# Kernel optimization log

Measured on AMD Instinct MI355X. Metric: run time of the kernel, lower is better.

Reference implementation:

```python
import jax, jax.numpy as jnp
import numpy as np

BLKQ = 64
BLKK = 64
TOPK_RATIO = 0.125


def setup_inputs() -> dict:
    key = jax.random.key(0)
    ks = jax.random.split(key, 4)
    B, L, H, D = 1, 4096, 16, 64
    q = jax.random.normal(ks[0], (B, L, H, D), jnp.float32)
    k = jax.random.normal(ks[1], (B, L, H, D), jnp.float32)
    v = jax.random.normal(ks[2], (B, L, H, D), jnp.float32)
    w_proj = jax.random.normal(ks[3], (D, D), jnp.float32) * 0.02
    b_proj = jnp.zeros((D,), jnp.float32)
    return {"q": q, "k": k, "v": v, "w_proj": w_proj, "b_proj": b_proj}


def _sparse_linear_attn(q, k, v, w_proj, b_proj):
    # q,k,v: (B, L, H, D) -> (B, H, L, D)
    q = jnp.transpose(q, (0, 2, 1, 3))
    k = jnp.transpose(k, (0, 2, 1, 3))
    v = jnp.transpose(v, (0, 2, 1, 3))
    B, H, L, D = q.shape
    M, N = L // BLKQ, L // BLKK  # L chosen divisible by block sizes (no padding)
    T = max(1, int(TOPK_RATIO * N))  # selected key blocks per query block

    qb = q.reshape(B, H, M, BLKQ, D)
    kb = k.reshape(B, H, N, BLKK, D)
    vb = v.reshape(B, H, N, BLKK, D)

    # --- block map: mean-pooled block descriptors, topk key blocks per query block ---
    qm = qb.mean(axis=3)  # (B,H,M,D)
    km = kb.mean(axis=3)  # (B,H,N,D)
    blk_scores = jnp.einsum('bhmd,bhnd->bhmn', qm, km)
    _, lut = jax.lax.top_k(blk_scores, T)  # (B,H,M,T) int32

    # --- gather selected K/V blocks ---
    b_idx = jnp.arange(B)[:, None, None, None]
    h_idx = jnp.arange(H)[None, :, None, None]
    k_sel = kb[b_idx, h_idx, lut]  # (B,H,M,T,BLKK,D)
    v_sel = vb[b_idx, h_idx, lut]  # (B,H,M,T,BLKK,D)

    # --- block-sparse softmax attention over gathered keys only ---
    scale = D ** (-0.5)
    att = jnp.einsum('bhmqd,bhmtkd->bhmqtk', qb, k_sel) * scale
    att = att.reshape(B, H, M, BLKQ, T * BLKK)
    p = jax.nn.softmax(att, axis=-1)
    o_s = jnp.einsum('bhmqn,bhmnd->bhmqd', p, v_sel.reshape(B, H, M, T * BLKK, D))
    o_s = o_s.reshape(B, H, L, D)

    # --- global linear attention with softmax feature map ---
    q_fm = jax.nn.softmax(q, axis=-1)
    k_fm = jax.nn.softmax(k, axis=-1)
    kvsum = jnp.einsum('bhld,bhle->bhde', k_fm, v)  # (B,H,D,D)
    ksum = k_fm.sum(axis=2)  # (B,H,D)
    num = jnp.einsum('bhld,bhde->bhle', q_fm, kvsum)
    den = jnp.einsum('bhld,bhd->bhl', q_fm, ksum)[..., None] + 1e-6
    o_l = num / den
    o_l = jnp.einsum('bhld,ed->bhle', o_l, w_proj) + b_proj  # nn.Linear: x @ W.T + b

    o = o_s + o_l
    return jnp.transpose(o, (0, 2, 1, 3))  # (B, L, H, D)


def reference(q, k, v, w_proj, b_proj):
    return _sparse_linear_attn(q, k, v, w_proj, b_proj)
```

## Files before the change

kernel.cpp:

```cpp
#include <hip/hip_runtime.h>


#define NH   16
#define DH   64
#define NBLK 64
#define TSEL 8

typedef unsigned short u16;
typedef unsigned int   u32;
typedef __attribute__((ext_vector_type(8))) short short8;
typedef __attribute__((ext_vector_type(4))) float f4;

#define MFMA_BF16(a, b, c) __builtin_amdgcn_mfma_f32_16x16x32_bf16(a, b, c, 0, 0, 0)

__device__ __forceinline__ u16 f2bf_rne(float f) {
  u32 u = __float_as_uint(f);
  u += 0x7fffu + ((u >> 16) & 1u);
  return (u16)(u >> 16);
}
__device__ __forceinline__ u32 pk2(float a, float b) {
  return (u32)f2bf_rne(a) | ((u32)f2bf_rne(b) << 16);
}
__device__ __forceinline__ float bf2f(u16 u) { return __uint_as_float(((u32)u) << 16); }

__device__ __forceinline__ short8 frag_row(const u16* t, int row, int jblk) {
  return *(const short8*)((const char*)t + row * 128 + ((jblk ^ (row & 7)) * 16));
}

__global__ __launch_bounds__(256) void prep_kernel(const float* __restrict__ q,
                                                   const float* __restrict__ k,
                                                   const float* __restrict__ v,
                                                   u16* __restrict__ kT,
                                                   u16* __restrict__ vT,
                                                   float* __restrict__ kvsum,
                                                   float* __restrict__ ksum,
                                                   float* __restrict__ kmv,
                                                   float* __restrict__ qkp) {
  __shared__ __align__(16) char vsl[8192];
  __shared__ __align__(16) char kfm[8192];
  __shared__ float redmx[256];
  __shared__ float redsm[256];
  __shared__ float ksred[256];
  int n = blockIdx.x, h = blockIdx.y, tid = threadIdx.x;
  int w = tid >> 6, lane = tid & 63;
  int row = lane, qd = w;
  int lq = lane & 15, quad = lane >> 4;

  float kv[16];
  {
    const float* kr = k + (size_t)(n * 64 + row) * 1024 + h * 64 + qd * 16;
#pragma unroll
    for (int c4 = 0; c4 < 4; c4++) {
      float4 a = *(const float4*)(kr + c4 * 4);
      kv[c4 * 4] = a.x; kv[c4 * 4 + 1] = a.y; kv[c4 * 4 + 2] = a.z; kv[c4 * 4 + 3] = a.w;
    }
  }
  {
    char* ktb = (char*)(kT + ((size_t)(h * 64 + n)) * 4096);
    uint4 w0 = make_uint4(pk2(kv[0], kv[1]), pk2(kv[2], kv[3]),
                          pk2(kv[4], kv[5]), pk2(kv[6], kv[7]));
    uint4 w1 = make_uint4(pk2(kv[8], kv[9]), pk2(kv[10], kv[11]),
                          pk2(kv[12], kv[13]), pk2(kv[14], kv[15]));
    *(uint4*)(ktb + row * 128 + (((2 * qd) ^ (row & 7)) * 16)) = w0;
    *(uint4*)(ktb + row * 128 + (((2 * qd + 1) ^ (row & 7)) * 16)) = w1;
  }
  {
    const float* vr = v + (size_t)(n * 64 + row) * 1024 + h * 64 + qd * 16;
    int kb = row >> 3, klo = row & 7;
#pragma unroll
    for (int c4 = 0; c4 < 4; c4++) {
      float4 a = *(const float4*)(vr + c4 * 4);
      float vv[4] = {a.x, a.y, a.z, a.w};
#pragma unroll
      for (int jj = 0; jj < 4; jj++) {
        int e = qd * 16 + c4 * 4 + jj;
        *(u16*)(vsl + e * 128 + ((kb ^ (e & 7)) * 16) + klo * 2) = f2bf_rne(vv[jj]);
      }
    }
  }
  {
    float kmval = 0.f;
#pragma unroll
    for (int j = 0; j < 16; j++) {
      float s = kv[j];
#pragma unroll
      for (int off = 1; off < 64; off <<= 1) s += __shfl_xor(s, off);
      if (lane == j) kmval = s;
    }
    if (lane < 16) kmv[h * 4096 + n * 64 + qd * 16 + lane] = kmval * (1.0f / 64.0f);
  }
  {
    float mx = kv[0];
#pragma unroll
    for (int j = 1; j < 16; j++) mx = fmaxf(mx, kv[j]);
    redmx[qd * 64 + row] = mx;
  }
  __syncthreads();
  {
    float mx = fmaxf(fmaxf(redmx[row], redmx[64 + row]),
                     fmaxf(redmx[128 + row], redmx[192 + row]));
    float sm = 0.f;
#pragma unroll
    for (int j = 0; j < 16; j++) { kv[j] = __expf(kv[j] - mx); sm += kv[j]; }
    redsm[qd * 64 + row] = sm;
  }
  __syncthreads();
  {
    float sm = redsm[row] + redsm[64 + row] + redsm[128 + row] + redsm[192 + row];
    float inv = 1.0f / sm;
    int rb = row >> 3, rlo = row & 7;
#pragma unroll
    for (int j = 0; j < 16; j++) {
      int d = qd * 16 + j;
      *(u16*)(kfm + d * 128 + (((rb) ^ (d & 7)) * 16) + rlo * 2) = f2bf_rne(kv[j] * inv);
    }
  }
  __syncthreads();

  {
    uint4* vt_out = (uint4*)(vT + ((size_t)(h * 64 + n)) * 4096);
    vt_out[tid] = ((const uint4*)vsl)[tid];
    vt_out[256 + tid] = ((const uint4*)vsl)[256 + tid];
  }
  {
    float ks = 0.f;
    short8 x0 = frag_row((const u16*)kfm, lane, 2 * w);
    short8 x1 = frag_row((const u16*)kfm, lane, 2 * w + 1);
#pragma unroll
    for (int e = 0; e < 8; e++) ks += bf2f((u16)x0[e]) + bf2f((u16)x1[e]);
    ksred[tid] = ks;
  }
  {
    f4 acc[4];
    f4 zz = {0.f, 0.f, 0.f, 0.f};
#pragma unroll
    for (int et = 0; et < 4; et++) acc[et] = zz;
#pragma unroll
    for (int ks2 = 0; ks2 < 2; ks2++) {
      short8 a_ = frag_row((const u16*)kfm, w * 16 + lq, 4 * ks2 + quad);
#pragma unroll
      for (int et = 0; et < 4; et++)
        acc[et] = MFMA_BF16(a_, frag_row((const u16*)vsl, et * 16 + lq, 4 * ks2 + quad), acc[et]);
    }
#pragma unroll
    for (int et = 0; et < 4; et++)
#pragma unroll
      for (int r = 0; r < 4; r++)
        atomicAdd(&kvsum[h * 4096 + (w * 16 + quad * 4 + r) * 64 + et * 16 + lq],
                  acc[et][r]);
  }
  __syncthreads();
  if (tid < 64)
    atomicAdd(&ksum[h * 64 + tid], ksred[tid] + ksred[64 + tid] +
                                   ksred[128 + tid] + ksred[192 + tid]);

  if (h < 4) {
    const float* base = q + ((size_t)(n * 64 + h * 16)) * 1024 + tid * 4;
    float4 acc = {0.f, 0.f, 0.f, 0.f};
#pragma unroll
    for (int i = 0; i < 16; i++) {
      float4 a = *(const float4*)(base + (size_t)i * 1024);
      acc.x += a.x; acc.y += a.y; acc.z += a.z; acc.w += a.w;
    }
    *(float4*)(qkp + ((size_t)(h * 64 + n)) * 1024 + tid * 4) = acc;
  }
}

__global__ __launch_bounds__(256) void post_kernel(const float* __restrict__ qkp,
                                                   const float* __restrict__ kmv,
                                                   const float* __restrict__ kvsum,
                                                   const float* __restrict__ wgt,
                                                   int* __restrict__ lut,
                                                   u16* __restrict__ m2t) {
  __shared__ float kv_s[64 * 65];
  __shared__ float w_s[64 * 65];
  __shared__ __align__(16) float qr_s[4][80];
  int bx = blockIdx.x, tid = threadIdx.x;
  if (bx < 256) {
    int h = bx >> 4, w = tid >> 6, n = tid & 63;
    int m = (bx & 15) * 4 + w;
    float qsum = 0.f;
#pragma unroll
    for (int rs = 0; rs < 4; rs++)
      qsum += qkp[((size_t)(rs * 64 + m)) * 1024 + h * 64 + n];
    qr_s[w][n] = qsum;
    __syncthreads();
    const float* kr = kmv + h * 4096 + n * 64;
    float s = 0.f;
#pragma unroll
    for (int d = 0; d < 64; d += 4) {
      float4 a = *(const float4*)(kr + d);
      float4 b = *(const float4*)(&qr_s[w][d]);
      s += a.x * b.x + a.y * b.y + a.z * b.z + a.w * b.w;
    }
    float my = s;
    for (int t = 0; t < TSEL; t++) {
      float v = my; int idx = n;
#pragma unroll
      for (int off = 1; off < 64; off <<= 1) {
        float ov = __shfl_xor(v, off);
        int oi = __shfl_xor(idx, off);
        if (ov > v || (ov == v && oi < idx)) { v = ov; idx = oi; }
      }
      if (n == 0) lut[(h * NBLK + m) * TSEL + t] = idx;
      if (n == idx) my = -INFINITY;
    }
  } else {
    int h = bx - 256;
#pragma unroll
    for (int jj = 0; jj < 16; jj++) {
      int idx = jj * 256 + tid;
      kv_s[(idx >> 6) * 65 + (idx & 63)] = kvsum[h * 4096 + idx];
      w_s[(idx >> 6) * 65 + (idx & 63)] = wgt[idx];
    }
    __syncthreads();
    int d = tid >> 2, e0 = (tid & 3) * 16;
    float acc[16];
#pragma unroll
    for (int e = 0; e < 16; e++) acc[e] = 0.f;
    for (int j = 0; j < 64; j++) {
      float kvj = kv_s[d * 65 + j];
#pragma unroll
      for (int e = 0; e < 16; e++)
        acc[e] = fmaf(kvj, w_s[(e0 + e) * 65 + j], acc[e]);
    }
    char* base = (char*)m2t + (size_t)h * 8192;
#pragma unroll
    for (int e = 0; e < 16; e++) {
      int ee = e0 + e;
      *(u16*)(base + ee * 128 + (((d >> 3) ^ (ee & 7)) * 16) + (d & 7) * 2) = f2bf_rne(acc[e]);
    }
  }
}

__global__ __launch_bounds__(256, 4) void fused_attn_kernel(const float* __restrict__ q,
                                                            const u16* __restrict__ kT,
                                                            const u16* __restrict__ vT,
                                                            const int* __restrict__ lut,
                                                            const u16* __restrict__ m2t,
                                                            const float* __restrict__ ksum,
                                                            const float* __restrict__ bproj,
                                                            float* __restrict__ out) {
  __shared__ __align__(16) char smem[33280];
  int m = blockIdx.x, h = blockIdx.y;
  int tid = threadIdx.x, w = tid >> 6, lane = tid & 63;
  int lq = lane & 15, quad = lane >> 4;
  u16* q_l = (u16*)smem;
  char* buf = smem + 8192;
  char* p_b = smem + 24576 + w * 2048;
  float* ks_s = (float*)(smem + 32768);
  float* b_s = (float*)(smem + 33024);

  const int lb = (h * NBLK + m) * TSEL;
  int blks[8];
#pragma unroll
  for (int t = 0; t < 8; t++) blks[t] = lut[lb + t];

  {
#pragma unroll
    for (int c = 0; c < 2; c++) {
      int lo = c * 4096 + tid * 16;
      int r = lo >> 7;
      int j = ((lo >> 4) & 7) ^ (r & 7);
      const float* gp = q + ((size_t)(m * 64 + r)) * 1024 + h * 64 + j * 8;
      float4 a = *(const float4*)gp;
      float4 b = *(const float4*)(gp + 4);
      *(uint4*)(smem + lo) = make_uint4(pk2(a.x, a.y), pk2(a.z, a.w),
                                        pk2(b.x, b.y), pk2(b.z, b.w));
    }
  }
  {
    const uint4* kt0 = (const uint4*)(kT + ((size_t)(h * 64 + blks[0])) * 4096);
    const uint4* vt0 = (const uint4*)(vT + ((size_t)(h * 64 + blks[0])) * 4096);
    ((uint4*)buf)[tid] = kt0[tid];
    ((uint4*)buf)[256 + tid] = kt0[256 + tid];
    ((uint4*)(buf + 8192))[tid] = vt0[tid];
    ((uint4*)(buf + 8192))[256 + tid] = vt0[256 + tid];
    if (tid < 64) { ks_s[tid] = ksum[h * 64 + tid]; b_s[tid] = bproj[tid]; }
  }
  __syncthreads();

  const int qrow = w * 16 + lq;
  short8 qf[2];
#pragma unroll
  for (int ks = 0; ks < 2; ks++) qf[ks] = frag_row(q_l, qrow, 4 * ks + quad);

  float mrun = -INFINITY, lrun = 0.f;
  f4 o[4];
  f4 zz = {0.f, 0.f, 0.f, 0.f};
#pragma unroll
  for (int et = 0; et < 4; et++) o[et] = zz;

  const u16* kc = (const u16*)buf;
  const u16* vc = (const u16*)(buf + 8192);

  for (int t = 0; t < 8; t++) {
    uint4 pk0, pk1, pv0, pv1;
    if (t < 7) {
      const uint4* ktn = (const uint4*)(kT + ((size_t)(h * 64 + blks[t + 1])) * 4096);
      const uint4* vtn = (const uint4*)(vT + ((size_t)(h * 64 + blks[t + 1])) * 4096);
      pk0 = ktn[tid]; pk1 = ktn[256 + tid];
      pv0 = vtn[tid]; pv1 = vtn[256 + tid];
    }

    f4 s[4];
#pragma unroll
    for (int kt = 0; kt < 4; kt++) s[kt] = zz;
#pragma unroll
    for (int ks = 0; ks < 2; ks++)
#pragma unroll
      for (int kt = 0; kt < 4; kt++)
        s[kt] = MFMA_BF16(frag_row(kc, kt * 16 + lq, 4 * ks + quad), qf[ks], s[kt]);

    float mp = -INFINITY;
#pragma unroll
    for (int kt = 0; kt < 4; kt++)
#pragma unroll
      for (int r = 0; r < 4; r++) mp = fmaxf(mp, s[kt][r]);
    mp = fmaxf(mp, __shfl_xor(mp, 16));
    mp = fmaxf(mp, __shfl_xor(mp, 32));
    mp *= 0.125f;
    float mn = fmaxf(mrun, mp);
    float al = __expf(mrun - mn);
    mrun = mn;
    float rs_ = 0.f;
#pragma unroll
    for (int kt = 0; kt < 4; kt++) {
      float p0 = __expf(fmaf(s[kt][0], 0.125f, -mn));
      float p1 = __expf(fmaf(s[kt][1], 0.125f, -mn));
      float p2 = __expf(fmaf(s[kt][2], 0.125f, -mn));
      float p3 = __expf(fmaf(s[kt][3], 0.125f, -mn));
      rs_ += p0 + p1 + p2 + p3;
      u32 lo32 = (__float_as_uint(p0) >> 16) | (__float_as_uint(p1) & 0xffff0000u);
      u32 hi32 = (__float_as_uint(p2) >> 16) | (__float_as_uint(p3) & 0xffff0000u);
      int addr = lq * 128 + (((kt * 2 + (quad >> 1)) ^ (lq & 7)) * 16) + (quad & 1) * 8;
      *(uint2*)(p_b + addr) = make_uint2(lo32, hi32);
    }
    rs_ += __shfl_xor(rs_, 16);
    rs_ += __shfl_xor(rs_, 32);
    lrun = lrun * al + rs_;
#pragma unroll
    for (int et = 0; et < 4; et++)
#pragma unroll
      for (int r = 0; r < 4; r++) o[et][r] *= al;

#pragma unroll
    for (int ks = 0; ks < 2; ks++) {
      short8 pf = frag_row((const u16*)p_b, lq, 4 * ks + quad);
#pragma unroll
      for (int et = 0; et < 4; et++)
        o[et] = MFMA_BF16(frag_row(vc, et * 16 + lq, 4 * ks + quad), pf, o[et]);
    }

    if (t < 7) {
      __syncthreads();
      ((uint4*)buf)[tid] = pk0;
      ((uint4*)buf)[256 + tid] = pk1;
      ((uint4*)(buf + 8192))[tid] = pv0;
      ((uint4*)(buf + 8192))[256 + tid] = pv1;
      __syncthreads();
    }
  }

  __syncthreads();
  {
    const uint4* src = (const uint4*)((const char*)m2t + (size_t)h * 8192);
    ((uint4*)buf)[tid] = src[tid];
    ((uint4*)buf)[256 + tid] = src[256 + tid];
  }
  __syncthreads();
  u16* m2_l = (u16*)buf;

  short8 qa = frag_row(q_l, qrow, 2 * quad);
  short8 qb = frag_row(q_l, qrow, 2 * quad + 1);
  float ev[16];
  float mx = -INFINITY;
#pragma unroll
  for (int j = 0; j < 8; j++) { float x = bf2f((u16)qa[j]); ev[j] = x; mx = fmaxf(mx, x); }
#pragma unroll
  for (int j = 0; j < 8; j++) { float x = bf2f((u16)qb[j]); ev[8 + j] = x; mx = fmaxf(mx, x); }
  mx = fmaxf(mx, __shfl_xor(mx, 16));
  mx = fmaxf(mx, __shfl_xor(mx, 32));
  float sum = 0.f, eks = 0.f;
#pragma unroll
  for (int j = 0; j < 16; j++) {
    float e = __expf(ev[j] - mx);
    ev[j] = e;
    sum += e;
    eks += e * ks_s[quad * 16 + j];
  }
  sum += __shfl_xor(sum, 16); sum += __shfl_xor(sum, 32);
  eks += __shfl_xor(eks, 16); eks += __shfl_xor(eks, 32);
  float invs = 1.0f / sum;
  float den = fmaf(eks, invs, 1e-6f);
  float scale = invs / den;
  uint4 e0v = make_uint4(pk2(ev[0], ev[1]), pk2(ev[2], ev[3]),
                         pk2(ev[4], ev[5]), pk2(ev[6], ev[7]));
  uint4 e1v = make_uint4(pk2(ev[8], ev[9]), pk2(ev[10], ev[11]),
                         pk2(ev[12], ev[13]), pk2(ev[14], ev[15]));
  *(uint4*)(p_b + lq * 128 + (((2 * quad) ^ (lq & 7)) * 16)) = e0v;
  *(uint4*)(p_b + lq * 128 + (((2 * quad + 1) ^ (lq & 7)) * 16)) = e1v;

  f4 oc[4];
#pragma unroll
  for (int et = 0; et < 4; et++) oc[et] = zz;
#pragma unroll
  for (int ks2 = 0; ks2 < 2; ks2++) {
    short8 ef = frag_row((const u16*)p_b, lq, 4 * ks2 + quad);
#pragma unroll
    for (int et = 0; et < 4; et++)
      oc[et] = MFMA_BF16(frag_row(m2_l, et * 16 + lq, 4 * ks2 + quad), ef, oc[et]);
  }

  float invl = 1.0f / lrun;
  float* gp = out + ((size_t)(m * 64 + qrow)) * 1024 + h * 64 + quad * 4;
#pragma unroll
  for (int et = 0; et < 4; et++) {
    int e0 = et * 16 + quad * 4;
    float4 ov;
    ov.x = o[et][0] * invl + oc[et][0] * scale + b_s[e0 + 0];
    ov.y = o[et][1] * invl + oc[et][1] * scale + b_s[e0 + 1];
    ov.z = o[et][2] * invl + oc[et][2] * scale + b_s[e0 + 2];
    ov.w = o[et][3] * invl + oc[et][3] * scale + b_s[e0 + 3];
    *(float4*)(gp + et * 16) = ov;
  }
}

extern "C" void kernel_launch(void* const* d_in, const int* in_sizes, int n_in,
                              void* d_out, int out_size, void* d_ws, size_t ws_size,
                              hipStream_t stream) {
  const float* q = (const float*)d_in[0];
  const float* k = (const float*)d_in[1];
  const float* v = (const float*)d_in[2];
  const float* w = (const float*)d_in[3];
  const float* b = (const float*)d_in[4];
  float* out = (float*)d_out;

  u16* kT = (u16*)d_ws;
  u16* vT = kT + 4194304;
  float* qkp = (float*)(vT + 4194304);
  float* kmv = qkp + 262144;
  int* lut = (int*)(kmv + 65536);
  float* kvsum = (float*)(lut + 8192);
  float* ksum = kvsum + 65536;
  u16* m2t = (u16*)(ksum + 1024);

  hipMemsetAsync(kvsum, 0, (65536 + 1024) * sizeof(float), stream);
  prep_kernel<<<dim3(64, 16), 256, 0, stream>>>(q, k, v, kT, vT, kvsum, ksum, kmv, qkp);
  post_kernel<<<272, 256, 0, stream>>>(qkp, kmv, kvsum, w, lut, m2t);
  fused_attn_kernel<<<dim3(64, 16), 256, 0, stream>>>(q, kT, vT, lut, m2t, ksum, b, out);
}
```

Measured before the change: 154.8 us.

## Rebalance prep/post work, remap block order, lazy softmax rescale, MFMA priority hints

The q-block pooling work, previously done only by blocks with h<4, is now spread across all prep blocks with smaller partial sums, and post reduces more partials. The k-mean shuffle reductions are replaced by an LDS transpose-and-sum. The kvsum×W projection is split across four blocks per head with float4 weight reads. A flat 1D grid with a head/block remap places heads across XCDs. The attention kernel skips the online-softmax rescale when no lane's max increases, wraps its MFMA sections in s_setprio, and trims LDS so it can target five blocks per CU. Together these aim to cut load imbalance, shuffle cost and occupancy limits, at the cost of more partial-sum traffic and extra LDS in prep.

```diff
diff --git a/kernel.cpp b/kernel.cpp
--- a/kernel.cpp
+++ b/kernel.cpp
@@ -35,13 +35,18 @@
                                                    float* __restrict__ kvsum,
                                                    float* __restrict__ ksum,
                                                    float* __restrict__ kmv,
-                                                   float* __restrict__ qkp) {
+                                                   float* __restrict__ qkp2) {
   __shared__ __align__(16) char vsl[8192];
   __shared__ __align__(16) char kfm[8192];
+  __shared__ float kcol[64 * 65];
   __shared__ float redmx[256];
   __shared__ float redsm[256];
+  __shared__ float kmred[256];
   __shared__ float ksred[256];
-  int n = blockIdx.x, h = blockIdx.y, tid = threadIdx.x;
+  int b = blockIdx.x;
+  int n = (b >> 3) & 63;
+  int h = 2 * (b & 7) + (b >> 9);
+  int tid = threadIdx.x;
   int w = tid >> 6, lane = tid & 63;
   int row = lane, qd = w;
   int lq = lane & 15, quad = lane >> 4;
@@ -65,6 +70,10 @@
     *(uint4*)(ktb + row * 128 + (((2 * qd + 1) ^ (row & 7)) * 16)) = w1;
   }
   {
+#pragma unroll
+    for (int j = 0; j < 16; j++) kcol[(qd * 16 + j) * 65 + row] = kv[j];
+  }
+  {
     const float* vr = v + (size_t)(n * 64 + row) * 1024 + h * 64 + qd * 16;
     int kb = row >> 3, klo = row & 7;
 #pragma unroll
@@ -79,23 +88,19 @@
     }
   }
   {
-    float kmval = 0.f;
-#pragma unroll
-    for (int j = 0; j < 16; j++) {
-      float s = kv[j];
-#pragma unroll
-      for (int off = 1; off < 64; off <<= 1) s += __shfl_xor(s, off);
-      if (lane == j) kmval = s;
-    }
-    if (lane < 16) kmv[h * 4096 + n * 64 + qd * 16 + lane] = kmval * (1.0f / 64.0f);
-  }
-  {
     float mx = kv[0];
 #pragma unroll
     for (int j = 1; j < 16; j++) mx = fmaxf(mx, kv[j]);
     redmx[qd * 64 + row] = mx;
   }
   __syncthreads();
+  {
+    int c = tid & 63, g = tid >> 6;
+    float pk = 0.f;
+#pragma unroll
+    for (int i = 0; i < 16; i++) pk += kcol[c * 65 + g * 16 + i];
+    kmred[g * 64 + c] = pk;
+  }
   {
     float mx = fmaxf(fmaxf(redmx[row], redmx[64 + row]),
                      fmaxf(redmx[128 + row], redmx[192 + row]));
@@ -105,6 +110,9 @@
     redsm[qd * 64 + row] = sm;
   }
   __syncthreads();
+  if (tid < 64)
+    kmv[h * 4096 + n * 64 + tid] =
+        (kmred[tid] + kmred[64 + tid] + kmred[128 + tid] + kmred[192 + tid]) * (1.0f / 64.0f);
   {
     float sm = redsm[row] + redsm[64 + row] + redsm[128 + row] + redsm[192 + row];
     float inv = 1.0f / sm;
@@ -154,26 +162,26 @@
     atomicAdd(&ksum[h * 64 + tid], ksred[tid] + ksred[64 + tid] +
                                    ksred[128 + tid] + ksred[192 + tid]);
 
-  if (h < 4) {
-    const float* base = q + ((size_t)(n * 64 + h * 16)) * 1024 + tid * 4;
+  {
+    const float* base = q + ((size_t)(n * 64 + h * 4)) * 1024 + tid * 4;
     float4 acc = {0.f, 0.f, 0.f, 0.f};
 #pragma unroll
-    for (int i = 0; i < 16; i++) {
+    for (int i = 0; i < 4; i++) {
       float4 a = *(const float4*)(base + (size_t)i * 1024);
       acc.x += a.x; acc.y += a.y; acc.z += a.z; acc.w += a.w;
     }
-    *(float4*)(qkp + ((size_t)(h * 64 + n)) * 1024 + tid * 4) = acc;
-  }
-}
-
-__global__ __launch_bounds__(256) void post_kernel(const float* __restrict__ qkp,
+    *(float4*)(qkp2 + ((size_t)(h * 64 + n)) * 1024 + tid * 4) = acc;
+  }
+}
+
+__global__ __launch_bounds__(256) void post_kernel(const float* __restrict__ qkp2,
                                                    const float* __restrict__ kmv,
                                                    const float* __restrict__ kvsum,
                                                    const float* __restrict__ wgt,
                                                    int* __restrict__ lut,
                                                    u16* __restrict__ m2t) {
   __shared__ float kv_s[64 * 65];
-  __shared__ float w_s[64 * 65];
+  __shared__ __align__(16) float wt[64 * 20];
   __shared__ __align__(16) float qr_s[4][80];
   int bx = blockIdx.x, tid = threadIdx.x;
   if (bx < 256) {
@@ -181,8 +189,8 @@
     int m = (bx & 15) * 4 + w;
     float qsum = 0.f;
 #pragma unroll
-    for (int rs = 0; rs < 4; rs++)
-      qsum += qkp[((size_t)(rs * 64 + m)) * 1024 + h * 64 + n];
+    for (int jg = 0; jg < 16; jg++)
+      qsum += qkp2[((size_t)(jg * 64 + m)) * 1024 + h * 64 + n];
     qr_s[w][n] = qsum;
     __syncthreads();
     const float* kr = kmv + h * 4096 + n * 64;
@@ -190,50 +198,55 @@
 #pragma unroll
     for (int d = 0; d < 64; d += 4) {
       float4 a = *(const float4*)(kr + d);
-      float4 b = *(const float4*)(&qr_s[w][d]);
-      s += a.x * b.x + a.y * b.y + a.z * b.z + a.w * b.w;
+      float4 bb = *(const float4*)(&qr_s[w][d]);
+      s += a.x * bb.x + a.y * bb.y + a.z * bb.z + a.w * bb.w;
     }
     float my = s;
     for (int t = 0; t < TSEL; t++) {
-      float v = my; int idx = n;
+      float vv = my; int idx = n;
 #pragma unroll
       for (int off = 1; off < 64; off <<= 1) {
-        float ov = __shfl_xor(v, off);
+        float ov = __shfl_xor(vv, off);
         int oi = __shfl_xor(idx, off);
-        if (ov > v || (ov == v && oi < idx)) { v = ov; idx = oi; }
+        if (ov > vv || (ov == vv && oi < idx)) { vv = ov; idx = oi; }
       }
       if (n == 0) lut[(h * NBLK + m) * TSEL + t] = idx;
       if (n == idx) my = -INFINITY;
     }
   } else {
-    int h = bx - 256;
+    int ib = bx - 256, h = ib >> 2, eq = ib & 3;
 #pragma unroll
     for (int jj = 0; jj < 16; jj++) {
-      int idx = jj * 256 + tid;
-      kv_s[(idx >> 6) * 65 + (idx & 63)] = kvsum[h * 4096 + idx];
-      w_s[(idx >> 6) * 65 + (idx & 63)] = wgt[idx];
+      int id2 = jj * 256 + tid;
+      kv_s[(id2 >> 6) * 65 + (id2 & 63)] = kvsum[h * 4096 + id2];
+    }
+#pragma unroll
+    for (int i = 0; i < 4; i++) {
+      int f = i * 256 + tid;
+      wt[(f & 63) * 20 + (f >> 6)] = wgt[(eq * 16 + (f >> 6)) * 64 + (f & 63)];
     }
     __syncthreads();
-    int d = tid >> 2, e0 = (tid & 3) * 16;
-    float acc[16];
-#pragma unroll
-    for (int e = 0; e < 16; e++) acc[e] = 0.f;
-    for (int j = 0; j < 64; j++) {
-      float kvj = kv_s[d * 65 + j];
-#pragma unroll
-      for (int e = 0; e < 16; e++)
-        acc[e] = fmaf(kvj, w_s[(e0 + e) * 65 + j], acc[e]);
+    int d = tid & 63, g = tid >> 6;
+    float4 acc = {0.f, 0.f, 0.f, 0.f};
+    for (int jj = 0; jj < 64; jj++) {
+      float kvj = kv_s[d * 65 + jj];
+      float4 wv = *(const float4*)(&wt[jj * 20 + g * 4]);
+      acc.x = fmaf(kvj, wv.x, acc.x);
+      acc.y = fmaf(kvj, wv.y, acc.y);
+      acc.z = fmaf(kvj, wv.z, acc.z);
+      acc.w = fmaf(kvj, wv.w, acc.w);
     }
     char* base = (char*)m2t + (size_t)h * 8192;
-#pragma unroll
-    for (int e = 0; e < 16; e++) {
-      int ee = e0 + e;
-      *(u16*)(base + ee * 128 + (((d >> 3) ^ (ee & 7)) * 16) + (d & 7) * 2) = f2bf_rne(acc[e]);
-    }
-  }
-}
-
-__global__ __launch_bounds__(256, 4) void fused_attn_kernel(const float* __restrict__ q,
+    float av[4] = {acc.x, acc.y, acc.z, acc.w};
+#pragma unroll
+    for (int c = 0; c < 4; c++) {
+      int ee = eq * 16 + g * 4 + c;
+      *(u16*)(base + ee * 128 + (((d >> 3) ^ (ee & 7)) * 16) + (d & 7) * 2) = f2bf_rne(av[c]);
+    }
+  }
+}
+
+__global__ __launch_bounds__(256, 5) void fused_attn_kernel(const float* __restrict__ q,
                                                             const u16* __restrict__ kT,
                                                             const u16* __restrict__ vT,
                                                             const int* __restrict__ lut,
@@ -241,15 +254,15 @@
                                                             const float* __restrict__ ksum,
                                                             const float* __restrict__ bproj,
                                                             float* __restrict__ out) {
-  __shared__ __align__(16) char smem[33280];
-  int m = blockIdx.x, h = blockIdx.y;
+  __shared__ __align__(16) char smem[32768];
+  int b = blockIdx.x;
+  int m = (b >> 3) & 63;
+  int h = 2 * (b & 7) + (b >> 9);
   int tid = threadIdx.x, w = tid >> 6, lane = tid & 63;
   int lq = lane & 15, quad = lane >> 4;
   u16* q_l = (u16*)smem;
   char* buf = smem + 8192;
   char* p_b = smem + 24576 + w * 2048;
-  float* ks_s = (float*)(smem + 32768);
-  float* b_s = (float*)(smem + 33024);
 
   const int lb = (h * NBLK + m) * TSEL;
   int blks[8];
@@ -264,9 +277,9 @@
       int j = ((lo >> 4) & 7) ^ (r & 7);
       const float* gp = q + ((size_t)(m * 64 + r)) * 1024 + h * 64 + j * 8;
       float4 a = *(const float4*)gp;
-      float4 b = *(const float4*)(gp + 4);
+      float4 bb = *(const float4*)(gp + 4);
       *(uint4*)(smem + lo) = make_uint4(pk2(a.x, a.y), pk2(a.z, a.w),
-                                        pk2(b.x, b.y), pk2(b.z, b.w));
+                                        pk2(bb.x, bb.y), pk2(bb.z, bb.w));
     }
   }
   {
@@ -276,7 +289,6 @@
     ((uint4*)buf)[256 + tid] = kt0[256 + tid];
     ((uint4*)(buf + 8192))[tid] = vt0[tid];
     ((uint4*)(buf + 8192))[256 + tid] = vt0[256 + tid];
-    if (tid < 64) { ks_s[tid] = ksum[h * 64 + tid]; b_s[tid] = bproj[tid]; }
   }
   __syncthreads();
 
@@ -306,11 +318,13 @@
     f4 s[4];
 #pragma unroll
     for (int kt = 0; kt < 4; kt++) s[kt] = zz;
+    __builtin_amdgcn_s_setprio(1);
 #pragma unroll
     for (int ks = 0; ks < 2; ks++)
 #pragma unroll
       for (int kt = 0; kt < 4; kt++)
         s[kt] = MFMA_BF16(frag_row(kc, kt * 16 + lq, 4 * ks + quad), qf[ks], s[kt]);
+    __builtin_amdgcn_s_setprio(0);
 
     float mp = -INFINITY;
 #pragma unroll
@@ -320,16 +334,23 @@
     mp = fmaxf(mp, __shfl_xor(mp, 16));
     mp = fmaxf(mp, __shfl_xor(mp, 32));
     mp *= 0.125f;
-    float mn = fmaxf(mrun, mp);
-    float al = __expf(mrun - mn);
-    mrun = mn;
+    if (__any(mp > mrun)) {
+      float mn = fmaxf(mrun, mp);
+      float al = __expf(mrun - mn);
+      mrun = mn;
+      lrun *= al;
+#pragma unroll
+      for (int et = 0; et < 4; et++)
+#pragma unroll
+        for (int r = 0; r < 4; r++) o[et][r] *= al;
+    }
     float rs_ = 0.f;
 #pragma unroll
     for (int kt = 0; kt < 4; kt++) {
-      float p0 = __expf(fmaf(s[kt][0], 0.125f, -mn));
-      float p1 = __expf(fmaf(s[kt][1], 0.125f, -mn));
-      float p2 = __expf(fmaf(s[kt][2], 0.125f, -mn));
-      float p3 = __expf(fmaf(s[kt][3], 0.125f, -mn));
+      float p0 = __expf(fmaf(s[kt][0], 0.125f, -mrun));
+      float p1 = __expf(fmaf(s[kt][1], 0.125f, -mrun));
+      float p2 = __expf(fmaf(s[kt][2], 0.125f, -mrun));
+      float p3 = __expf(fmaf(s[kt][3], 0.125f, -mrun));
       rs_ += p0 + p1 + p2 + p3;
       u32 lo32 = (__float_as_uint(p0) >> 16) | (__float_as_uint(p1) & 0xffff0000u);
       u32 hi32 = (__float_as_uint(p2) >> 16) | (__float_as_uint(p3) & 0xffff0000u);
@@ -338,12 +359,9 @@
     }
     rs_ += __shfl_xor(rs_, 16);
     rs_ += __shfl_xor(rs_, 32);
-    lrun = lrun * al + rs_;
-#pragma unroll
-    for (int et = 0; et < 4; et++)
-#pragma unroll
-      for (int r = 0; r < 4; r++) o[et][r] *= al;
-
+    lrun += rs_;
+
+    __builtin_amdgcn_s_setprio(1);
 #pragma unroll
     for (int ks = 0; ks < 2; ks++) {
       short8 pf = frag_row((const u16*)p_b, lq, 4 * ks + quad);
@@ -351,6 +369,7 @@
       for (int et = 0; et < 4; et++)
         o[et] = MFMA_BF16(frag_row(vc, et * 16 + lq, 4 * ks + quad), pf, o[et]);
     }
+    __builtin_amdgcn_s_setprio(0);
 
     if (t < 7) {
       __syncthreads();
@@ -367,9 +386,15 @@
     const uint4* src = (const uint4*)((const char*)m2t + (size_t)h * 8192);
     ((uint4*)buf)[tid] = src[tid];
     ((uint4*)buf)[256 + tid] = src[256 + tid];
+    if (tid < 64) {
+      ((float*)(buf + 8192))[tid] = ksum[h * 64 + tid];
+      ((float*)(buf + 8448))[tid] = bproj[tid];
+    }
   }
   __syncthreads();
   u16* m2_l = (u16*)buf;
+  float* ks_s = (float*)(buf + 8192);
+  float* b_s = (float*)(buf + 8448);
 
   short8 qa = frag_row(q_l, qrow, 2 * quad);
   short8 qb = frag_row(q_l, qrow, 2 * quad + 1);
@@ -402,8 +427,10 @@
   *(uint4*)(p_b + lq * 128 + (((2 * quad + 1) ^ (lq & 7)) * 16)) = e1v;
 
   f4 oc[4];
-#pragma unroll
-  for (int et = 0; et < 4; et++) oc[et] = zz;
+  f4 zz2 = {0.f, 0.f, 0.f, 0.f};
+#pragma unroll
+  for (int et = 0; et < 4; et++) oc[et] = zz2;
+  __builtin_amdgcn_s_setprio(1);
 #pragma unroll
   for (int ks2 = 0; ks2 < 2; ks2++) {
     short8 ef = frag_row((const u16*)p_b, lq, 4 * ks2 + quad);
@@ -411,6 +438,7 @@
     for (int et = 0; et < 4; et++)
       oc[et] = MFMA_BF16(frag_row(m2_l, et * 16 + lq, 4 * ks2 + quad), ef, oc[et]);
   }
+  __builtin_amdgcn_s_setprio(0);
 
   float invl = 1.0f / lrun;
   float* gp = out + ((size_t)(m * 64 + qrow)) * 1024 + h * 64 + quad * 4;
@@ -438,15 +466,15 @@
 
   u16* kT = (u16*)d_ws;
   u16* vT = kT + 4194304;
-  float* qkp = (float*)(vT + 4194304);
-  float* kmv = qkp + 262144;
+  float* qkp2 = (float*)(vT + 4194304);
+  float* kmv = qkp2 + 1048576;
   int* lut = (int*)(kmv + 65536);
   float* kvsum = (float*)(lut + 8192);
   float* ksum = kvsum + 65536;
   u16* m2t = (u16*)(ksum + 1024);
 
   hipMemsetAsync(kvsum, 0, (65536 + 1024) * sizeof(float), stream);
-  prep_kernel<<<dim3(64, 16), 256, 0, stream>>>(q, k, v, kT, vT, kvsum, ksum, kmv, qkp);
-  post_kernel<<<272, 256, 0, stream>>>(qkp, kmv, kvsum, w, lut, m2t);
-  fused_attn_kernel<<<dim3(64, 16), 256, 0, stream>>>(q, kT, vT, lut, m2t, ksum, b, out);
-}
+  prep_kernel<<<1024, 256, 0, stream>>>(q, k, v, kT, vT, kvsum, ksum, kmv, qkp2);
+  post_kernel<<<320, 256, 0, stream>>>(qkp2, kmv, kvsum, w, lut, m2t);
+  fused_attn_kernel<<<1024, 256, 0, stream>>>(q, kT, vT, lut, m2t, ksum, b, out);
+}
```

Result: faster. 146.7 us (-5.2%).
